# Kernel tuning notes

Measured on AMD Instinct MI355X. Metric: run time of the kernel, lower is better.

Reference implementation:

```python
import jax, jax.numpy as jnp
import numpy as np

B, S, H = 2, 1024, 2048
KD = 32
N_CACHE = 16
RANKS = (4, 12, 40, 128)
SIM_THRESH = 0.95
CRIT_T, SIMPLE_T = 0.8, 0.3
EPS = 1e-8


def setup_inputs() -> dict:
    key = jax.random.key(0)
    ks = jax.random.split(key, 24)
    f32 = jnp.float32
    inp = {}
    inp['hidden_states'] = jax.random.normal(ks[0], (B, S, H), f32)
    # token importance scorer: Linear(H, H//4) -> ReLU -> Linear(H//4, 1)
    inp['scorer_w1'] = jax.random.normal(ks[1], (H // 4, H), f32) * 0.1
    inp['scorer_b1'] = jnp.zeros((H // 4,), f32)
    inp['scorer_w2'] = jax.random.normal(ks[2], (1, H // 4), f32) * 0.1
    inp['scorer_b2'] = jnp.zeros((1,), f32)
    inp['pos_importance'] = jnp.ones((1024,), f32)
    # orthogonal key projection [KD, H] (rows orthonormal)
    q, _ = jnp.linalg.qr(jax.random.normal(ks[3], (H, KD), f32))
    inp['key_proj_w'] = q.T
    # cached keys: per-batch-row L2-normalized then flattened, as in _compute_key
    ck = jax.random.normal(ks[4], (N_CACHE, B, KD), f32)
    ck = ck / jnp.linalg.norm(ck, axis=-1, keepdims=True)
    inp['cache_keys'] = ck.reshape(N_CACHE, B * KD)
    inp['cache_deltas'] = jax.random.normal(ks[5], (N_CACHE, B, S, H), f32) * 0.02
    # complexity estimator: Linear(H, 64) -> ReLU -> Linear(64, 4)
    inp['ce_w1'] = jax.random.normal(ks[6], (64, H), f32) * 0.02
    inp['ce_b1'] = jnp.zeros((64,), f32)
    inp['ce_w2'] = jax.random.normal(ks[7], (len(RANKS), 64), f32) * 0.02
    inp['ce_b2'] = jnp.zeros((len(RANKS),), f32)
    # adaptive low-rank U/V per rank option, init std=0.02
    for i, r in enumerate(RANKS):
        inp[f'u{r}'] = jax.random.normal(ks[8 + 2 * i], (r, H), f32) * 0.02
        inp[f'v{r}'] = jax.random.normal(ks[9 + 2 * i], (H, r), f32) * 0.02
    # dense stand-in for the wrapped original transformer layer
    inp['layer_w'] = jax.random.normal(ks[16], (H, H), f32) * 0.02
    inp['layer_b'] = jnp.zeros((H,), f32)
    return inp


def _forward(hidden_states, scorer_w1, scorer_b1, scorer_w2, scorer_b2,
             pos_importance, key_proj_w, cache_keys, cache_deltas,
             ce_w1, ce_b1, ce_w2, ce_b2,
             u4, v4, u12, v12, u40, v40, u128, v128,
             layer_w, layer_b):
    x = hidden_states
    Bn, Sn, _ = x.shape
    # ---- token importance scoring ----
    h = jax.nn.relu(jnp.einsum('bsh,fh->bsf', x, scorer_w1) + scorer_b1)
    content = jnp.einsum('bsf,of->bso', h, scorer_w2)[..., 0] + scorer_b2[0]  # [B,S]
    pos = pos_importance[:Sn][None, :]
    imp = jax.nn.sigmoid(content + 0.1 * pos)
    imp = imp.at[:, 0].multiply(2.0).at[:, -1].multiply(2.0)
    critical = imp > CRIT_T
    simple = imp < SIMPLE_T
    normal = ~(critical | simple)
    # ---- critical path: original layer on critically-masked input ----
    crit_in = jnp.where(critical[..., None], x, 0.0)
    crit_out = jnp.einsum('bsh,oh->bso', crit_in, layer_w) + layer_b
    # ---- simple path: batched 1-NN cosine cache lookup (replaces python loop) ----
    x_pooled = x.mean(axis=1)  # [B,H]
    qk = jax.lax.stop_gradient(x_pooled @ key_proj_w.T)  # no_grad in original
    qk = qk / jnp.maximum(jnp.linalg.norm(qk, axis=-1, keepdims=True), EPS)
    qf = qk.reshape(-1)  # flattened [B*KD], as F.cosine_similarity(dim=0)
    ck = jax.lax.stop_gradient(cache_keys)  # cached entries are detached
    sims = (ck @ qf) / (jnp.maximum(jnp.linalg.norm(ck, axis=-1), EPS)
                        * jnp.maximum(jnp.linalg.norm(qf), EPS))  # [N_CACHE]
    best = jnp.argmax(sims)
    hit = sims[best] >= SIM_THRESH
    cached_delta = jax.lax.stop_gradient(cache_deltas[best])  # [B,S,H]
    lr4 = (x @ u4.T) @ v4.T  # rank-4 update on cache miss
    simple_out = x + jnp.where(hit, cached_delta, lr4)
    # ---- normal path: adaptive-rank low-rank update ----
    ce_h = jax.nn.relu(jax.lax.stop_gradient(x_pooled) @ ce_w1.T + ce_b1)
    scores = ce_h @ ce_w2.T + ce_b2  # [B,4]
    rank_idx = jnp.argmax(scores.reshape(-1)) % len(RANKS)  # flat argmax as torch.argmax
    branches = [
        lambda xx: (xx @ u4.T) @ v4.T,
        lambda xx: (xx @ u12.T) @ v12.T,
        lambda xx: (xx @ u40.T) @ v40.T,
        lambda xx: (xx @ u128.T) @ v128.T,
    ]
    normal_update = jax.lax.switch(rank_idx, branches, x)
    normal_out = x + normal_update
    # ---- route per-token (masks partition all tokens) ----
    out = jnp.where(critical[..., None], crit_out,
          jnp.where(simple[..., None], simple_out, normal_out))
    return out


def reference(hidden_states, scorer_w1, scorer_b1, scorer_w2, scorer_b2,
              pos_importance, key_proj_w, cache_keys, cache_deltas,
              ce_w1, ce_b1, ce_w2, ce_b2,
              u4, v4, u12, v12, u40, v40, u128, v128,
              layer_w, layer_b):
    return _forward(hidden_states, scorer_w1, scorer_b1, scorer_w2, scorer_b2,
                    pos_importance, key_proj_w, cache_keys, cache_deltas,
                    ce_w1, ce_b1, ce_w2, ce_b2,
                    u4, v4, u12, v12, u40, v40, u128, v128,
                    layer_w, layer_b)
```

## Files before the change

kernel.cpp:

```cpp
#include <hip/hip_runtime.h>
#include <math.h>

#define B_  2
#define S_  1024
#define H_  2048
#define F_  512
#define KD_ 32
#define NC_ 16
#define M_  2048
#define NPROJ 184
#define LDP 192

typedef __attribute__((ext_vector_type(8))) short bf16x8;
typedef __attribute__((ext_vector_type(4))) float f32x4;

typedef __attribute__((address_space(1))) const void gvoid_t;
typedef __attribute__((address_space(3))) void lvoid_t;

__device__ __forceinline__ void gld16(const void* g, void* l) {
    __builtin_amdgcn_global_load_lds((gvoid_t*)g, (lvoid_t*)l, 16, 0, 0);
}

__device__ __forceinline__ ushort f2bf(float f) {
    unsigned u = __float_as_uint(f);
    u += 0x7FFFu + ((u >> 16) & 1u);
    return (ushort)(u >> 16);
}
__device__ __forceinline__ float bf2f(ushort h) {
    return __uint_as_float(((unsigned)h) << 16);
}
__device__ __forceinline__ uint4 pack_hi8(float4 a, float4 b) {
    uint4 r;
    r.x = (unsigned)f2bf(a.x) | ((unsigned)f2bf(a.y) << 16);
    r.y = (unsigned)f2bf(a.z) | ((unsigned)f2bf(a.w) << 16);
    r.z = (unsigned)f2bf(b.x) | ((unsigned)f2bf(b.y) << 16);
    r.w = (unsigned)f2bf(b.z) | ((unsigned)f2bf(b.w) << 16);
    return r;
}
__device__ __forceinline__ void pack_hilo8(float4 a, float4 b, uint4* hi, uint4* lo) {
    float v[8] = {a.x, a.y, a.z, a.w, b.x, b.y, b.z, b.w};
    unsigned h[8], l[8];
#pragma unroll
    for (int i = 0; i < 8; ++i) {
        ushort hh = f2bf(v[i]);
        h[i] = hh;
        l[i] = f2bf(v[i] - bf2f(hh));
    }
    *hi = make_uint4(h[0] | (h[1] << 16), h[2] | (h[3] << 16),
                     h[4] | (h[5] << 16), h[6] | (h[7] << 16));
    *lo = make_uint4(l[0] | (l[1] << 16), l[2] | (l[3] << 16),
                     l[4] | (l[5] << 16), l[6] | (l[7] << 16));
}

__global__ __launch_bounds__(256) void conv_kernel(
    const float* __restrict__ x, const float* __restrict__ lw,
    const float* __restrict__ sw1,
    const float* __restrict__ u4, const float* __restrict__ u12,
    const float* __restrict__ u40, const float* __restrict__ u128,
    ushort* __restrict__ xhi, ushort* __restrict__ xlo,
    ushort* __restrict__ lwh, ushort* __restrict__ swh,
    ushort* __restrict__ swl, ushort* __restrict__ ubh,
    float* __restrict__ partial) {
    int blk = blockIdx.x, tid = threadIdx.x;
    if (blk < 128) {
        int c0 = tid << 3;
        float cs0 = 0.f, cs1 = 0.f, cs2 = 0.f, cs3 = 0.f;
        float cs4 = 0.f, cs5 = 0.f, cs6 = 0.f, cs7 = 0.f;
        for (int r = 0; r < 16; ++r) {
            size_t off = (size_t)(blk * 16 + r) * H_ + c0;
            float4 a = *(const float4*)(x + off);
            float4 b = *(const float4*)(x + off + 4);
            cs0 += a.x; cs1 += a.y; cs2 += a.z; cs3 += a.w;
            cs4 += b.x; cs5 += b.y; cs6 += b.z; cs7 += b.w;
            uint4 hi, lo;
            pack_hilo8(a, b, &hi, &lo);
            *(uint4*)(xhi + off) = hi;
            *(uint4*)(xlo + off) = lo;
        }
        float* pr = partial + (size_t)blk * H_ + c0;
        pr[0] = cs0; pr[1] = cs1; pr[2] = cs2; pr[3] = cs3;
        pr[4] = cs4; pr[5] = cs5; pr[6] = cs6; pr[7] = cs7;
    } else if (blk < 1152) {
        size_t base = (size_t)(blk - 128) * 4096 + (size_t)tid * 16;
#pragma unroll
        for (int q = 0; q < 2; ++q) {
            size_t o = base + q * 8;
            float4 a = *(const float4*)(lw + o);
            float4 b = *(const float4*)(lw + o + 4);
            *(uint4*)(lwh + o) = pack_hi8(a, b);
        }
    } else if (blk < 1408) {
        size_t base = (size_t)(blk - 1152) * 4096 + (size_t)tid * 16;
#pragma unroll
        for (int q = 0; q < 2; ++q) {
            size_t o = base + q * 8;
            float4 a = *(const float4*)(sw1 + o);
            float4 b = *(const float4*)(sw1 + o + 4);
            uint4 hi, lo;
            pack_hilo8(a, b, &hi, &lo);
            *(uint4*)(swh + o) = hi;
            *(uint4*)(swl + o) = lo;
        }
    } else {
        const float* src; ushort* dst; int rel;
        if (blk < 1410)      { src = u4;   dst = ubh;            rel = blk - 1408; }
        else if (blk < 1416) { src = u12;  dst = ubh + 4 * H_;   rel = blk - 1410; }
        else if (blk < 1436) { src = u40;  dst = ubh + 16 * H_;  rel = blk - 1416; }
        else                 { src = u128; dst = ubh + 56 * H_;  rel = blk - 1436; }
        size_t base = (size_t)rel * 4096 + (size_t)tid * 16;
#pragma unroll
        for (int q = 0; q < 2; ++q) {
            size_t o = base + q * 8;
            float4 a = *(const float4*)(src + o);
            float4 b = *(const float4*)(src + o + 4);
            *(uint4*)(dst + o) = pack_hi8(a, b);
        }
    }
}

__global__ __launch_bounds__(256) void pool_final_kernel(
    const float* __restrict__ partial, float* __restrict__ xp) {
    int b = blockIdx.x >> 3, chunk = blockIdx.x & 7;
    int col = (chunk << 8) + threadIdx.x;
    float s = 0.f;
    for (int seg = 0; seg < 64; ++seg)
        s += partial[(size_t)(b * 64 + seg) * H_ + col];
    xp[b * H_ + col] = s * (1.0f / S_);
}

__global__ __launch_bounds__(256) void decide_dots(
    const float* __restrict__ xp, const float* __restrict__ kpw,
    const float* __restrict__ cw1, float* __restrict__ dots) {
    __shared__ float red[4];
    int o = blockIdx.x, tid = threadIdx.x;
    const float* xr;
    const float* wr;
    if (o < 64) {
        xr = xp + (o >> 5) * H_;
        wr = kpw + (size_t)(o & 31) * H_;
    } else {
        int o2 = o - 64;
        xr = xp + (o2 >> 6) * H_;
        wr = cw1 + (size_t)(o2 & 63) * H_;
    }
    int k0 = tid << 3;
    float4 xa = *(const float4*)(xr + k0);
    float4 xb = *(const float4*)(xr + k0 + 4);
    float4 wa = *(const float4*)(wr + k0);
    float4 wb = *(const float4*)(wr + k0 + 4);
    float s = xa.x * wa.x + xa.y * wa.y + xa.z * wa.z + xa.w * wa.w
            + xb.x * wb.x + xb.y * wb.y + xb.z * wb.z + xb.w * wb.w;
    for (int off = 32; off > 0; off >>= 1) s += __shfl_down(s, off, 64);
    if ((tid & 63) == 0) red[tid >> 6] = s;
    __syncthreads();
    if (tid == 0) dots[o] = red[0] + red[1] + red[2] + red[3];
}

__global__ __launch_bounds__(64) void decide_final(
    const float* __restrict__ dots, const float* __restrict__ ck,
    const float* __restrict__ cb1, const float* __restrict__ cw2,
    const float* __restrict__ cb2, int* __restrict__ flags) {
    __shared__ float qk_s[64], ce_s[128], sims_s[NC_], sc_s[8];
    __shared__ float qn_s;
    int tid = threadIdx.x;
    if (tid < 64) qk_s[tid] = dots[tid];
    if (tid < 64) {
        ce_s[tid]      = fmaxf(dots[64 + tid] + cb1[tid & 63], 0.f);
        ce_s[tid + 64] = fmaxf(dots[128 + tid] + cb1[tid & 63], 0.f);
    }
    __syncthreads();
    if (tid == 0) {
        for (int b = 0; b < B_; ++b) {
            float nn = 0.f;
            for (int d = 0; d < KD_; ++d) { float v = qk_s[b * KD_ + d]; nn += v * v; }
            float den = fmaxf(sqrtf(nn), 1e-8f);
            for (int d = 0; d < KD_; ++d) qk_s[b * KD_ + d] /= den;
        }
        float qn = 0.f;
        for (int i = 0; i < B_ * KD_; ++i) qn += qk_s[i] * qk_s[i];
        qn_s = fmaxf(sqrtf(qn), 1e-8f);
    }
    __syncthreads();
    if (tid < NC_) {
        float dot = 0.f, nn = 0.f;
        for (int i = 0; i < B_ * KD_; ++i) {
            float c = ck[tid * (B_ * KD_) + i];
            dot += c * qk_s[i]; nn += c * c;
        }
        sims_s[tid] = dot / (fmaxf(sqrtf(nn), 1e-8f) * qn_s);
    }
    if (tid >= 32 && tid < 40) {
        int p = tid - 32, b = p >> 2, o = p & 3;
        float v = cb2[o];
        for (int j = 0; j < 64; ++j) v += ce_s[b * 64 + j] * cw2[o * 64 + j];
        sc_s[p] = v;
    }
    __syncthreads();
    if (tid == 0) {
        float bestv = -1e30f; int best = 0;
        for (int n = 0; n < NC_; ++n)
            if (sims_s[n] > bestv) { bestv = sims_s[n]; best = n; }
        flags[2] = (bestv >= 0.95f) ? 1 : 0;
        flags[3] = best;
        float bs = -1e30f; int bi = 0;
        for (int p = 0; p < 8; ++p)
            if (sc_s[p] > bs) { bs = sc_s[p]; bi = p; }
        flags[1] = bi & 3;
    }
}

__global__ __launch_bounds__(256) void big_gemm(
    const ushort* __restrict__ xhi, const ushort* __restrict__ xlo,
    const ushort* __restrict__ swh, const ushort* __restrict__ swl,
    const ushort* __restrict__ ubh,
    float* __restrict__ Hp, float* __restrict__ Pp) {
    __shared__ ushort Ah[128][32], Al[128][32], Bh[128][32], Bl[128][32];
    int m0 = blockIdx.x << 7;
    int ny = blockIdx.y;
    int kz = blockIdx.z;
    bool split = ny < 4;
    int tid = threadIdx.x;
    int lr = tid >> 2;
    int lc = (tid & 3) << 3;

    const ushort* a0p = xhi + (size_t)(m0 + lr) * H_ + lc;
    const ushort* a1p = a0p + (size_t)64 * H_;
    const ushort* l0p = xlo + (size_t)(m0 + lr) * H_ + lc;
    const ushort* l1p = l0p + (size_t)64 * H_;
    const ushort* b0p; const ushort* b1p;
    const ushort* c0p = l0p; const ushort* c1p = l1p;
    if (split) {
        b0p = swh + (size_t)(ny * 128 + lr) * H_ + lc;
        b1p = b0p + (size_t)64 * H_;
        c0p = swl + (size_t)(ny * 128 + lr) * H_ + lc;
        c1p = c0p + (size_t)64 * H_;
    } else {
        b0p = ubh + (size_t)((ny - 4) * 128 + lr) * H_ + lc;
        b1p = b0p + (size_t)64 * H_;
    }
    ushort* Ad0 = &Ah[lr][lc];      ushort* Ad1 = &Ah[lr + 64][lc];
    ushort* Ld0 = &Al[lr][lc];      ushort* Ld1 = &Al[lr + 64][lc];
    ushort* Bd0 = &Bh[lr][lc];      ushort* Bd1 = &Bh[lr + 64][lc];
    ushort* Cd0 = &Bl[lr][lc];      ushort* Cd1 = &Bl[lr + 64][lc];

    int lane = tid & 63, w = tid >> 6;
    int wm = (w >> 1) << 6, wn = (w & 1) << 6;
    int fr = lane & 15, kb = (lane >> 4) << 3;

    f32x4 zero4 = {0.f, 0.f, 0.f, 0.f};
    f32x4 acc[4][4];
#pragma unroll
    for (int i = 0; i < 4; ++i)
#pragma unroll
        for (int j = 0; j < 4; ++j) acc[i][j] = zero4;

    int kbeg = kz << 10;
    for (int kt = 0; kt < 32; ++kt) {
        int k0 = kbeg + (kt << 5);
        gld16(a0p + k0, Ad0); gld16(a1p + k0, Ad1);
        gld16(b0p + k0, Bd0); gld16(b1p + k0, Bd1);
        if (split) {
            gld16(l0p + k0, Ld0); gld16(l1p + k0, Ld1);
            gld16(c0p + k0, Cd0); gld16(c1p + k0, Cd1);
        }
        __syncthreads();
        bf16x8 ah[4], bh4[4], al4[4], bl4[4];
#pragma unroll
        for (int mt = 0; mt < 4; ++mt)
            ah[mt] = *(const bf16x8*)&Ah[wm + (mt << 4) + fr][kb];
#pragma unroll
        for (int nt = 0; nt < 4; ++nt)
            bh4[nt] = *(const bf16x8*)&Bh[wn + (nt << 4) + fr][kb];
        if (split) {
#pragma unroll
            for (int mt = 0; mt < 4; ++mt)
                al4[mt] = *(const bf16x8*)&Al[wm + (mt << 4) + fr][kb];
#pragma unroll
            for (int nt = 0; nt < 4; ++nt)
                bl4[nt] = *(const bf16x8*)&Bl[wn + (nt << 4) + fr][kb];
        }
#pragma unroll
        for (int mt = 0; mt < 4; ++mt)
#pragma unroll
            for (int nt = 0; nt < 4; ++nt) {
                acc[mt][nt] = __builtin_amdgcn_mfma_f32_16x16x32_bf16(
                    ah[mt], bh4[nt], acc[mt][nt], 0, 0, 0);
                if (split) {
                    acc[mt][nt] = __builtin_amdgcn_mfma_f32_16x16x32_bf16(
                        ah[mt], bl4[nt], acc[mt][nt], 0, 0, 0);
                    acc[mt][nt] = __builtin_amdgcn_mfma_f32_16x16x32_bf16(
                        al4[mt], bh4[nt], acc[mt][nt], 0, 0, 0);
                }
            }
        __syncthreads();
    }

    int orr = (lane >> 4) << 2;
    if (split) {
        float* dst = Hp + (size_t)kz * M_ * F_;
#pragma unroll
        for (int mt = 0; mt < 4; ++mt)
#pragma unroll
            for (int r = 0; r < 4; ++r) {
                int m = m0 + wm + (mt << 4) + orr + r;
                float* cr = dst + (size_t)m * F_ + (ny << 7) + wn;
#pragma unroll
                for (int nt = 0; nt < 4; ++nt)
                    cr[(nt << 4) + fr] = acc[mt][nt][r];
            }
    } else {
        float* dst = Pp + (size_t)kz * M_ * LDP;
        int nb0 = (ny - 4) << 7;
#pragma unroll
        for (int mt = 0; mt < 4; ++mt)
#pragma unroll
            for (int r = 0; r < 4; ++r) {
                int m = m0 + wm + (mt << 4) + orr + r;
                float* cr = dst + (size_t)m * LDP;
#pragma unroll
                for (int nt = 0; nt < 4; ++nt) {
                    int c = nb0 + wn + (nt << 4) + fr;
                    if (c < NPROJ) cr[c] = acc[mt][nt][r];
                }
            }
    }
}

__global__ __launch_bounds__(256) void route_kernel(
    const float* __restrict__ Hp, const float* __restrict__ sb1,
    const float* __restrict__ sw2, const float* __restrict__ sb2,
    const float* __restrict__ pos,
    int* __restrict__ flags, int* __restrict__ route, int* __restrict__ clist) {
    int tid = threadIdx.x;
    int m = (blockIdx.x << 2) + (tid >> 6);
    int lane = tid & 63;
    const float* h0 = Hp + (size_t)m * F_;
    const float* h1 = Hp + (size_t)M_ * F_ + (size_t)m * F_;
    float s = 0.f;
    for (int f = lane; f < F_; f += 64)
        s += fmaxf(h0[f] + h1[f] + sb1[f], 0.f) * sw2[f];
    for (int off = 32; off > 0; off >>= 1) s += __shfl_down(s, off, 64);
    if (lane == 0) {
        float content = s + sb2[0];
        int si = m & (S_ - 1);
        float imp = 1.0f / (1.0f + expf(-(content + 0.1f * pos[si])));
        if (si == 0 || si == S_ - 1) imp *= 2.0f;
        int rt = (imp > 0.8f) ? 0 : ((imp < 0.3f) ? 1 : 2);
        route[m] = rt;
        if (rt == 0) {
            int idx = atomicAdd(&flags[0], 1);
            clist[idx] = m;
        }
    }
}

__global__ __launch_bounds__(256) void crit_gemm(
    const ushort* __restrict__ xhi, const ushort* __restrict__ lwh,
    const float* __restrict__ lb, const int* __restrict__ clist,
    const int* __restrict__ flags, float* __restrict__ out) {
    __shared__ ushort Ah[128][32], Bh[128][32];
    int M = flags[0];
    int m0 = blockIdx.x << 7;
    if (m0 >= M) return;
    int n0 = blockIdx.y << 7;
    int tid = threadIdx.x;
    int lr = tid >> 2, lc = (tid & 3) << 3;

    int gm0 = m0 + lr, gm1 = m0 + lr + 64;
    int ar0 = clist[gm0 < M ? gm0 : (M - 1)];
    int ar1 = clist[gm1 < M ? gm1 : (M - 1)];
    const ushort* a0p = xhi + (size_t)ar0 * H_ + lc;
    const ushort* a1p = xhi + (size_t)ar1 * H_ + lc;
    const ushort* b0p = lwh + (size_t)(n0 + lr) * H_ + lc;
    const ushort* b1p = b0p + (size_t)64 * H_;
    ushort* Ad0 = &Ah[lr][lc];  ushort* Ad1 = &Ah[lr + 64][lc];
    ushort* Bd0 = &Bh[lr][lc];  ushort* Bd1 = &Bh[lr + 64][lc];

    int lane = tid & 63, w = tid >> 6;
    int wm = (w >> 1) << 6, wn = (w & 1) << 6;
    int fr = lane & 15, kb = (lane >> 4) << 3;

    f32x4 zero4 = {0.f, 0.f, 0.f, 0.f};
    f32x4 acc[4][4];
#pragma unroll
    for (int i = 0; i < 4; ++i)
#pragma unroll
        for (int j = 0; j < 4; ++j) acc[i][j] = zero4;

    for (int kt = 0; kt < 64; ++kt) {
        int k0 = kt << 5;
        gld16(a0p + k0, Ad0); gld16(a1p + k0, Ad1);
        gld16(b0p + k0, Bd0); gld16(b1p + k0, Bd1);
        __syncthreads();
        bf16x8 af[4], bf4[4];
#pragma unroll
        for (int mt = 0; mt < 4; ++mt)
            af[mt] = *(const bf16x8*)&Ah[wm + (mt << 4) + fr][kb];
#pragma unroll
        for (int nt = 0; nt < 4; ++nt)
            bf4[nt] = *(const bf16x8*)&Bh[wn + (nt << 4) + fr][kb];
#pragma unroll
        for (int mt = 0; mt < 4; ++mt)
#pragma unroll
            for (int nt = 0; nt < 4; ++nt)
                acc[mt][nt] = __builtin_amdgcn_mfma_f32_16x16x32_bf16(
                    af[mt], bf4[nt], acc[mt][nt], 0, 0, 0);
        __syncthreads();
    }

    int orr = (lane >> 4) << 2;
#pragma unroll
    for (int mt = 0; mt < 4; ++mt)
#pragma unroll
        for (int r = 0; r < 4; ++r) {
            int m = m0 + wm + (mt << 4) + orr + r;
            if (m < M) {
                float* cr = out + (size_t)clist[m] * H_;
#pragma unroll
                for (int nt = 0; nt < 4; ++nt) {
                    int c = n0 + wn + (nt << 4) + fr;
                    cr[c] = acc[mt][nt][r] + lb[c];
                }
            }
        }
}

__global__ __launch_bounds__(256) void stage2_kernel(
    const float* __restrict__ x, const float* __restrict__ Pp,
    const float* __restrict__ v4, const float* __restrict__ v12,
    const float* __restrict__ v40, const float* __restrict__ v128,
    const float* __restrict__ cd, const int* __restrict__ flags,
    const int* __restrict__ route, float* __restrict__ out) {
    __shared__ float TsR[16][132];
    __shared__ float Ts4[16][4];
    __shared__ int rt_s[16];
    int tid = threadIdx.x;
    int m0 = (blockIdx.x >> 4) << 4;
    int c0 = (blockIdx.x & 15) << 7;

    if (tid < 16) rt_s[tid] = route[m0 + tid];
    int r = flags[1];
    const float* V = (r == 0) ? v4 : (r == 1) ? v12 : (r == 2) ? v40 : v128;
    int Kr  = (r == 0) ? 4 : (r == 1) ? 12 : (r == 2) ? 40 : 128;
    int off = (r == 0) ? 0 : (r == 1) ? 4  : (r == 2) ? 16 : 56;
    int hit = flags[2], best = flags[3];

    const float* Pp1 = Pp + (size_t)M_ * LDP;
    for (int idx = tid; idx < 16 * Kr; idx += 256) {
        int i = idx / Kr, j = idx - i * Kr;
        size_t o = (size_t)(m0 + i) * LDP + off + j;
        TsR[i][j] = Pp[o] + Pp1[o];
    }
    if (tid < 64) {
        int i = tid >> 2, j = tid & 3;
        size_t o = (size_t)(m0 + i) * LDP + j;
        Ts4[i][j] = Pp[o] + Pp1[o];
    }
    __syncthreads();
    bool any1 = false, any2 = false;
#pragma unroll
    for (int i = 0; i < 16; ++i) { any1 |= (rt_s[i] == 1); any2 |= (rt_s[i] == 2); }
    if (!any1 && !any2) return;
    bool need4 = any1 && !hit;

    int c = c0 + (tid & 127);
    int i0 = (tid >> 7) << 3;

    float aR[8];
#pragma unroll
    for (int i = 0; i < 8; ++i) aR[i] = 0.f;
    if (any2) {
        const float* vrow = V + (size_t)c * Kr;
        for (int j = 0; j < Kr; j += 4) {
            const float4 vv = *(const float4*)(vrow + j);
#pragma unroll
            for (int i = 0; i < 8; ++i) {
                const float4 tv = *(const float4*)&TsR[i0 + i][j];
                aR[i] += tv.x * vv.x + tv.y * vv.y + tv.z * vv.z + tv.w * vv.w;
            }
        }
    }
    float a4[8];
    if (need4) {
        const float4 vv = *(const float4*)(v4 + (size_t)c * 4);
#pragma unroll
        for (int i = 0; i < 8; ++i) {
            const float4 tv = *(const float4*)&Ts4[i0 + i][0];
            a4[i] = tv.x * vv.x + tv.y * vv.y + tv.z * vv.z + tv.w * vv.w;
        }
    }
#pragma unroll
    for (int i = 0; i < 8; ++i) {
        int rt = rt_s[i0 + i];
        if (rt == 0) continue;
        size_t o = (size_t)(m0 + i0 + i) * H_ + c;
        float upd;
        if (rt == 1)
            upd = hit ? cd[(size_t)best * (size_t)(M_ * H_) + o] : a4[i];
        else
            upd = aR[i];
        out[o] = x[o] + upd;
    }
}

extern "C" void kernel_launch(void* const* d_in, const int* in_sizes, int n_in,
                              void* d_out, int out_size, void* d_ws, size_t ws_size,
                              hipStream_t stream) {
    const float* x    = (const float*)d_in[0];
    const float* sw1  = (const float*)d_in[1];
    const float* sb1  = (const float*)d_in[2];
    const float* sw2  = (const float*)d_in[3];
    const float* sb2  = (const float*)d_in[4];
    const float* pos  = (const float*)d_in[5];
    const float* kpw  = (const float*)d_in[6];
    const float* ck   = (const float*)d_in[7];
    const float* cd   = (const float*)d_in[8];
    const float* cw1  = (const float*)d_in[9];
    const float* cb1  = (const float*)d_in[10];
    const float* cw2  = (const float*)d_in[11];
    const float* cb2  = (const float*)d_in[12];
    const float* u4   = (const float*)d_in[13];
    const float* v4   = (const float*)d_in[14];
    const float* u12  = (const float*)d_in[15];
    const float* v12  = (const float*)d_in[16];
    const float* u40  = (const float*)d_in[17];
    const float* v40  = (const float*)d_in[18];
    const float* u128 = (const float*)d_in[19];
    const float* v128 = (const float*)d_in[20];
    const float* lw   = (const float*)d_in[21];
    const float* lb   = (const float*)d_in[22];
    float* out = (float*)d_out;

    ushort* xhi = (ushort*)d_ws;
    ushort* xlo = xhi + (size_t)M_ * H_;
    ushort* lwh = xlo + (size_t)M_ * H_;
    ushort* swh = lwh + (size_t)H_ * H_;
    ushort* swl = swh + (size_t)F_ * H_;
    ushort* ubh = swl + (size_t)F_ * H_;
    float* fbase   = (float*)(ubh + (size_t)256 * H_);
    float* xp      = fbase;
    float* partial = xp + 2 * H_;
    float* Pp      = partial + 128 * H_;
    float* dots    = Pp + 2 * (size_t)M_ * LDP;
    int*   flags   = (int*)(dots + 256);
    int*   route   = flags + 8;
    int*   clist   = route + M_;
    float* Hp = out;

    hipMemsetAsync(flags, 0, sizeof(int), stream);

    conv_kernel<<<1500, 256, 0, stream>>>(x, lw, sw1, u4, u12, u40, u128,
                                          xhi, xlo, lwh, swh, swl, ubh, partial);
    pool_final_kernel<<<16, 256, 0, stream>>>(partial, xp);
    decide_dots<<<192, 256, 0, stream>>>(xp, kpw, cw1, dots);
    decide_final<<<1, 64, 0, stream>>>(dots, ck, cb1, cw2, cb2, flags);
    big_gemm<<<dim3(16, 6, 2), 256, 0, stream>>>(xhi, xlo, swh, swl, ubh, Hp, Pp);
    route_kernel<<<512, 256, 0, stream>>>(Hp, sb1, sw2, sb2, pos,
                                          flags, route, clist);
    crit_gemm<<<dim3(16, 16), 256, 0, stream>>>(xhi, lwh, lb, clist, flags, out);
    stage2_kernel<<<2048, 256, 0, stream>>>(x, Pp, v4, v12, v40, v128,
                                            cd, flags, route, out);
}
```

Before: 529.6 us.

## Double-buffer LDS in GEMMs and raise split-K to four for big_gemm

Adds double-buffered shared-memory tiles to big_gemm and crit_gemm, so the next K-tile's global-to-LDS loads are issued while MFMAs run on the current tile. big_gemm's split-K goes from 2 to 4 (grid z=4, 16 K-steps each) to run more blocks. The partial results move from the output buffer into a workspace region, and route_kernel and stage2 now sum four partials. This doubles LDS use per block and adds partial-sum traffic in exchange for more latency hiding and more parallelism.

New measurement: 519.0 us. 1.02x faster.

```diff
diff --git a/kernel.cpp b/kernel.cpp
--- a/kernel.cpp
+++ b/kernel.cpp
@@ -10,6 +10,7 @@
 #define M_  2048
 #define NPROJ 184
 #define LDP 192
+#define KZ_ 4
 
 typedef __attribute__((ext_vector_type(8))) short bf16x8;
 typedef __attribute__((ext_vector_type(4))) float f32x4;
@@ -214,7 +215,7 @@
     const ushort* __restrict__ swh, const ushort* __restrict__ swl,
     const ushort* __restrict__ ubh,
     float* __restrict__ Hp, float* __restrict__ Pp) {
-    __shared__ ushort Ah[128][32], Al[128][32], Bh[128][32], Bl[128][32];
+    __shared__ ushort Ah[2][128][32], Al[2][128][32], Bh[2][128][32], Bl[2][128][32];
     int m0 = blockIdx.x << 7;
     int ny = blockIdx.y;
     int kz = blockIdx.z;
@@ -238,10 +239,6 @@
         b0p = ubh + (size_t)((ny - 4) * 128 + lr) * H_ + lc;
         b1p = b0p + (size_t)64 * H_;
     }
-    ushort* Ad0 = &Ah[lr][lc];      ushort* Ad1 = &Ah[lr + 64][lc];
-    ushort* Ld0 = &Al[lr][lc];      ushort* Ld1 = &Al[lr + 64][lc];
-    ushort* Bd0 = &Bh[lr][lc];      ushort* Bd1 = &Bh[lr + 64][lc];
-    ushort* Cd0 = &Bl[lr][lc];      ushort* Cd1 = &Bl[lr + 64][lc];
 
     int lane = tid & 63, w = tid >> 6;
     int wm = (w >> 1) << 6, wn = (w & 1) << 6;
@@ -254,30 +251,41 @@
 #pragma unroll
         for (int j = 0; j < 4; ++j) acc[i][j] = zero4;
 
-    int kbeg = kz << 10;
-    for (int kt = 0; kt < 32; ++kt) {
-        int k0 = kbeg + (kt << 5);
-        gld16(a0p + k0, Ad0); gld16(a1p + k0, Ad1);
-        gld16(b0p + k0, Bd0); gld16(b1p + k0, Bd1);
+    int kbeg = kz << 9;
+
+#define STAGE_BG(bb, k0)                                                  \
+    do {                                                                  \
+        gld16(a0p + (k0), &Ah[bb][lr][lc]);                               \
+        gld16(a1p + (k0), &Ah[bb][lr + 64][lc]);                          \
+        gld16(b0p + (k0), &Bh[bb][lr][lc]);                               \
+        gld16(b1p + (k0), &Bh[bb][lr + 64][lc]);                          \
+        if (split) {                                                      \
+            gld16(l0p + (k0), &Al[bb][lr][lc]);                           \
+            gld16(l1p + (k0), &Al[bb][lr + 64][lc]);                      \
+            gld16(c0p + (k0), &Bl[bb][lr][lc]);                           \
+            gld16(c1p + (k0), &Bl[bb][lr + 64][lc]);                      \
+        }                                                                 \
+    } while (0)
+
+    STAGE_BG(0, kbeg);
+    __syncthreads();
+    int cur = 0;
+    for (int kt = 0; kt < 16; ++kt) {
+        if (kt + 1 < 16) STAGE_BG(cur ^ 1, kbeg + ((kt + 1) << 5));
+        bf16x8 ah[4], bh4[4], al4[4], bl4[4];
+#pragma unroll
+        for (int mt = 0; mt < 4; ++mt)
+            ah[mt] = *(const bf16x8*)&Ah[cur][wm + (mt << 4) + fr][kb];
+#pragma unroll
+        for (int nt = 0; nt < 4; ++nt)
+            bh4[nt] = *(const bf16x8*)&Bh[cur][wn + (nt << 4) + fr][kb];
         if (split) {
-            gld16(l0p + k0, Ld0); gld16(l1p + k0, Ld1);
-            gld16(c0p + k0, Cd0); gld16(c1p + k0, Cd1);
-        }
-        __syncthreads();
-        bf16x8 ah[4], bh4[4], al4[4], bl4[4];
-#pragma unroll
-        for (int mt = 0; mt < 4; ++mt)
-            ah[mt] = *(const bf16x8*)&Ah[wm + (mt << 4) + fr][kb];
-#pragma unroll
-        for (int nt = 0; nt < 4; ++nt)
-            bh4[nt] = *(const bf16x8*)&Bh[wn + (nt << 4) + fr][kb];
-        if (split) {
 #pragma unroll
             for (int mt = 0; mt < 4; ++mt)
-                al4[mt] = *(const bf16x8*)&Al[wm + (mt << 4) + fr][kb];
+                al4[mt] = *(const bf16x8*)&Al[cur][wm + (mt << 4) + fr][kb];
 #pragma unroll
             for (int nt = 0; nt < 4; ++nt)
-                bl4[nt] = *(const bf16x8*)&Bl[wn + (nt << 4) + fr][kb];
+                bl4[nt] = *(const bf16x8*)&Bl[cur][wn + (nt << 4) + fr][kb];
         }
 #pragma unroll
         for (int mt = 0; mt < 4; ++mt)
@@ -293,7 +301,9 @@
                 }
             }
         __syncthreads();
-    }
+        cur ^= 1;
+    }
+#undef STAGE_BG
 
     int orr = (lane >> 4) << 2;
     if (split) {
@@ -335,10 +345,12 @@
     int m = (blockIdx.x << 2) + (tid >> 6);
     int lane = tid & 63;
     const float* h0 = Hp + (size_t)m * F_;
-    const float* h1 = Hp + (size_t)M_ * F_ + (size_t)m * F_;
+    const float* h1 = h0 + (size_t)M_ * F_;
+    const float* h2 = h1 + (size_t)M_ * F_;
+    const float* h3 = h2 + (size_t)M_ * F_;
     float s = 0.f;
     for (int f = lane; f < F_; f += 64)
-        s += fmaxf(h0[f] + h1[f] + sb1[f], 0.f) * sw2[f];
+        s += fmaxf(h0[f] + h1[f] + h2[f] + h3[f] + sb1[f], 0.f) * sw2[f];
     for (int off = 32; off > 0; off >>= 1) s += __shfl_down(s, off, 64);
     if (lane == 0) {
         float content = s + sb2[0];
@@ -358,7 +370,7 @@
     const ushort* __restrict__ xhi, const ushort* __restrict__ lwh,
     const float* __restrict__ lb, const int* __restrict__ clist,
     const int* __restrict__ flags, float* __restrict__ out) {
-    __shared__ ushort Ah[128][32], Bh[128][32];
+    __shared__ ushort Ah[2][128][32], Bh[2][128][32];
     int M = flags[0];
     int m0 = blockIdx.x << 7;
     if (m0 >= M) return;
@@ -373,8 +385,6 @@
     const ushort* a1p = xhi + (size_t)ar1 * H_ + lc;
     const ushort* b0p = lwh + (size_t)(n0 + lr) * H_ + lc;
     const ushort* b1p = b0p + (size_t)64 * H_;
-    ushort* Ad0 = &Ah[lr][lc];  ushort* Ad1 = &Ah[lr + 64][lc];
-    ushort* Bd0 = &Bh[lr][lc];  ushort* Bd1 = &Bh[lr + 64][lc];
 
     int lane = tid & 63, w = tid >> 6;
     int wm = (w >> 1) << 6, wn = (w & 1) << 6;
@@ -387,18 +397,26 @@
 #pragma unroll
         for (int j = 0; j < 4; ++j) acc[i][j] = zero4;
 
+#define STAGE_CG(bb, k0)                                                  \
+    do {                                                                  \
+        gld16(a0p + (k0), &Ah[bb][lr][lc]);                               \
+        gld16(a1p + (k0), &Ah[bb][lr + 64][lc]);                          \
+        gld16(b0p + (k0), &Bh[bb][lr][lc]);                               \
+        gld16(b1p + (k0), &Bh[bb][lr + 64][lc]);                          \
+    } while (0)
+
+    STAGE_CG(0, 0);
+    __syncthreads();
+    int cur = 0;
     for (int kt = 0; kt < 64; ++kt) {
-        int k0 = kt << 5;
-        gld16(a0p + k0, Ad0); gld16(a1p + k0, Ad1);
-        gld16(b0p + k0, Bd0); gld16(b1p + k0, Bd1);
-        __syncthreads();
+        if (kt + 1 < 64) STAGE_CG(cur ^ 1, (kt + 1) << 5);
         bf16x8 af[4], bf4[4];
 #pragma unroll
         for (int mt = 0; mt < 4; ++mt)
-            af[mt] = *(const bf16x8*)&Ah[wm + (mt << 4) + fr][kb];
+            af[mt] = *(const bf16x8*)&Ah[cur][wm + (mt << 4) + fr][kb];
 #pragma unroll
         for (int nt = 0; nt < 4; ++nt)
-            bf4[nt] = *(const bf16x8*)&Bh[wn + (nt << 4) + fr][kb];
+            bf4[nt] = *(const bf16x8*)&Bh[cur][wn + (nt << 4) + fr][kb];
 #pragma unroll
         for (int mt = 0; mt < 4; ++mt)
 #pragma unroll
@@ -406,7 +424,9 @@
                 acc[mt][nt] = __builtin_amdgcn_mfma_f32_16x16x32_bf16(
                     af[mt], bf4[nt], acc[mt][nt], 0, 0, 0);
         __syncthreads();
-    }
+        cur ^= 1;
+    }
+#undef STAGE_CG
 
     int orr = (lane >> 4) << 2;
 #pragma unroll
@@ -446,15 +466,17 @@
     int hit = flags[2], best = flags[3];
 
     const float* Pp1 = Pp + (size_t)M_ * LDP;
+    const float* Pp2 = Pp1 + (size_t)M_ * LDP;
+    const float* Pp3 = Pp2 + (size_t)M_ * LDP;
     for (int idx = tid; idx < 16 * Kr; idx += 256) {
         int i = idx / Kr, j = idx - i * Kr;
         size_t o = (size_t)(m0 + i) * LDP + off + j;
-        TsR[i][j] = Pp[o] + Pp1[o];
+        TsR[i][j] = Pp[o] + Pp1[o] + Pp2[o] + Pp3[o];
     }
     if (tid < 64) {
         int i = tid >> 2, j = tid & 3;
         size_t o = (size_t)(m0 + i) * LDP + j;
-        Ts4[i][j] = Pp[o] + Pp1[o];
+        Ts4[i][j] = Pp[o] + Pp1[o] + Pp2[o] + Pp3[o];
     }
     __syncthreads();
     bool any1 = false, any2 = false;
@@ -541,11 +563,11 @@
     float* xp      = fbase;
     float* partial = xp + 2 * H_;
     float* Pp      = partial + 128 * H_;
-    float* dots    = Pp + 2 * (size_t)M_ * LDP;
+    float* Hp      = Pp + (size_t)KZ_ * M_ * LDP;
+    float* dots    = Hp + (size_t)KZ_ * M_ * F_;
     int*   flags   = (int*)(dots + 256);
     int*   route   = flags + 8;
     int*   clist   = route + M_;
-    float* Hp = out;
 
     hipMemsetAsync(flags, 0, sizeof(int), stream);
 
@@ -554,7 +576,7 @@
     pool_final_kernel<<<16, 256, 0, stream>>>(partial, xp);
     decide_dots<<<192, 256, 0, stream>>>(xp, kpw, cw1, dots);
     decide_final<<<1, 64, 0, stream>>>(dots, ck, cb1, cw2, cb2, flags);
-    big_gemm<<<dim3(16, 6, 2), 256, 0, stream>>>(xhi, xlo, swh, swl, ubh, Hp, Pp);
+    big_gemm<<<dim3(16, 6, KZ_), 256, 0, stream>>>(xhi, xlo, swh, swl, ubh, Hp, Pp);
     route_kernel<<<512, 256, 0, stream>>>(Hp, sb1, sw2, sb2, pos,
                                           flags, route, clist);
     crit_gemm<<<dim3(16, 16), 256, 0, stream>>>(xhi, lwh, lb, clist, flags, out);
```
